# Kernel tuning notes

Hardware: AMD Instinct MI355X
Metric: run time of the kernel (lower is better)

The kernel has to match this reference:

```python
import jax, jax.numpy as jnp
import numpy as np

QK_DIM = 1024
V_DIM = 1024
NUM_HEADS = 16
HEAD_DIM = 64
INNER = NUM_HEADS * HEAD_DIM  # 1024
SCALE = HEAD_DIM ** -0.5


def setup_inputs() -> dict:
    key = jax.random.key(0)
    ks = jax.random.split(key, 8)
    m, nq, nkv = 4, 2048, 2048
    xq = jax.random.normal(ks[0], (m, nq, QK_DIM), dtype=jnp.float32)
    xk = jax.random.normal(ks[1], (m, nkv, QK_DIM), dtype=jnp.float32)
    xv = jax.random.normal(ks[2], (m, nkv, V_DIM), dtype=jnp.float32)
    # torch nn.Linear weights are [out, in]; y = x @ W.T
    s_qk = (QK_DIM) ** -0.5
    s_in = (INNER) ** -0.5
    Wq = jax.random.uniform(ks[3], (INNER, QK_DIM), jnp.float32, -s_qk, s_qk)
    Wk = jax.random.uniform(ks[4], (INNER, QK_DIM), jnp.float32, -s_qk, s_qk)
    Wv = jax.random.uniform(ks[5], (INNER, V_DIM), jnp.float32, -s_qk, s_qk)
    Wo = jax.random.uniform(ks[6], (V_DIM, INNER), jnp.float32, -s_in, s_in)
    bo = jax.random.uniform(ks[7], (V_DIM,), jnp.float32, -s_in, s_in)
    return {"xq": xq, "xk": xk, "xv": xv, "Wq": Wq, "Wk": Wk, "Wv": Wv, "Wo": Wo, "bo": bo}


def reference(xq, xk, xv, Wq, Wk, Wv, Wo, bo):
    m, nq, _ = xq.shape
    nkv = xk.shape[1]
    # projections (no bias), split heads: b n (h d) -> b h n d
    q = (xq @ Wq.T).reshape(m, nq, NUM_HEADS, HEAD_DIM).transpose(0, 2, 1, 3)
    k = (xk @ Wk.T).reshape(m, nkv, NUM_HEADS, HEAD_DIM).transpose(0, 2, 1, 3)
    v = (xv @ Wv.T).reshape(m, nkv, NUM_HEADS, HEAD_DIM).transpose(0, 2, 1, 3)
    dots = jnp.einsum("bhqd,bhkd->bhqk", q, k) * SCALE  # [m,h,nq,nkv]
    attn = jax.nn.softmax(dots, axis=-1)
    out = jnp.einsum("bhqk,bhkd->bhqd", attn, v)
    out = out.transpose(0, 2, 1, 3).reshape(m, nq, INNER)  # b h n d -> b n (h d)
    return out @ Wo.T + bo  # to_out Linear (dropout p=0 -> identity)
```

## Files before the change

kernel.cpp:

```cpp
#include <hip/hip_runtime.h>

typedef unsigned short u16;
using bf16x8 = __attribute__((ext_vector_type(8))) __bf16;
using f32x4  = __attribute__((ext_vector_type(4))) float;

#define QSCALE 0.18033688011f

#define EXP2F(x) __builtin_amdgcn_exp2f(x)
#define SCHED_FENCE() __builtin_amdgcn_sched_barrier(0)

__device__ __forceinline__ u16 f2bf(float f) {
  union { float f; unsigned int u; } x; x.f = f;
  unsigned int r = x.u + 0x7FFFu + ((x.u >> 16) & 1u);
  return (u16)(r >> 16);
}

__device__ __forceinline__ bf16x8 ld8(const u16* p) {
  return *reinterpret_cast<const bf16x8*>(p);
}

__device__ __forceinline__ void gload16(const void* g, void* l) {
  __builtin_amdgcn_global_load_lds(
      (const __attribute__((address_space(1))) unsigned int*)g,
      (__attribute__((address_space(3))) unsigned int*)l, 16, 0, 0);
}

__global__ void cast3_f32_to_bf16(const float* __restrict__ a, const float* __restrict__ b,
                                  const float* __restrict__ c, u16* __restrict__ out, int n4) {
  const int y = blockIdx.y;
  const int i = blockIdx.x * 256 + threadIdx.x;
  if (i >= n4) return;
  const float* src = (y == 0) ? a : (y == 1) ? b : c;
  const float4 v = reinterpret_cast<const float4*>(src)[i];
  ushort4 o;
  o.x = f2bf(v.x); o.y = f2bf(v.y); o.z = f2bf(v.z); o.w = f2bf(v.w);
  reinterpret_cast<ushort4*>(out + (size_t)y * n4 * 4)[i] = o;
}

__global__ void cast4_f32_to_bf16(const float* __restrict__ a, const float* __restrict__ b,
                                  const float* __restrict__ c, const float* __restrict__ d,
                                  u16* __restrict__ out, int n4) {
  const int y = blockIdx.y;
  const int i = blockIdx.x * 256 + threadIdx.x;
  if (i >= n4) return;
  const float* src = (y == 0) ? a : (y == 1) ? b : (y == 2) ? c : d;
  const float4 v = reinterpret_cast<const float4*>(src)[i];
  ushort4 o;
  o.x = f2bf(v.x); o.y = f2bf(v.y); o.z = f2bf(v.z); o.w = f2bf(v.w);
  reinterpret_cast<ushort4*>(out + (size_t)y * n4 * 4)[i] = o;
}

#define GEMM_CORE(A_, B_, K_, BX_, BY_)                                              \
  __shared__ alignas(16) u16 lds_a[128 * 32];                                        \
  __shared__ alignas(16) u16 lds_b[128 * 32];                                        \
  const int t = threadIdx.x;                                                         \
  const int w = t >> 6, lane = t & 63;                                               \
  const int wr = w >> 1, wc = w & 1;                                                 \
  const size_t row0 = (size_t)(BY_) * 128;                                           \
  const size_t col0 = (size_t)(BX_) * 128;                                           \
  f32x4 acc[4][4];                                                                   \
  _Pragma("unroll") for (int i = 0; i < 4; ++i)                                      \
    _Pragma("unroll") for (int j = 0; j < 4; ++j) acc[i][j] = {0.f, 0.f, 0.f, 0.f};  \
  const u16* ga = A_ + (row0 + (t >> 2)) * K_ + (t & 3) * 8;                         \
  const u16* gb = B_ + (col0 + (t >> 2)) * K_ + (t & 3) * 8;                         \
  u16* la = lds_a + w * 512;                                                         \
  u16* lb = lds_b + w * 512;                                                         \
  const int fr = lane & 15;                                                          \
  const int fk = (lane >> 4) * 8;                                                    \
  for (int kt = 0; kt < K_; kt += 32) {                                              \
    __syncthreads();                                                                 \
    gload16(ga + kt, la);                                                            \
    gload16(ga + (size_t)64 * K_ + kt, la + 2048);                                   \
    gload16(gb + kt, lb);                                                            \
    gload16(gb + (size_t)64 * K_ + kt, lb + 2048);                                   \
    asm volatile("s_waitcnt vmcnt(0)" ::: "memory");                                 \
    __syncthreads();                                                                 \
    bf16x8 af[4], bfr[4];                                                            \
    _Pragma("unroll") for (int i = 0; i < 4; ++i)                                    \
      af[i] = ld8(&lds_a[(wr * 64 + i * 16 + fr) * 32 + fk]);                        \
    _Pragma("unroll") for (int j = 0; j < 4; ++j)                                    \
      bfr[j] = ld8(&lds_b[(wc * 64 + j * 16 + fr) * 32 + fk]);                       \
    _Pragma("unroll") for (int i = 0; i < 4; ++i)                                    \
      _Pragma("unroll") for (int j = 0; j < 4; ++j)                                  \
        acc[i][j] = __builtin_amdgcn_mfma_f32_16x16x32_bf16(af[i], bfr[j], acc[i][j], 0, 0, 0); \
  }                                                                                  \
  const int er = (lane >> 4) * 4, ec = lane & 15;

__device__ __forceinline__ void gemm8b_core(const u16* __restrict__ A, const u16* __restrict__ B,
                                            int by, int bx, f32x4 (&acc)[4][4],
                                            u16 (*lds_a)[8192], u16 (*lds_b)[16384]) {
  const int t = threadIdx.x;
  const int w = t >> 6, lane = t & 63;
  const int wm = w >> 2, wn = w & 3;
  const int fr = lane & 15, lh = lane >> 4;
  const int xr = (fr & 4) << 2;
  const int kch = ((t & 7) ^ ((t >> 4) & 2)) * 8;

  const u16* ga = A + (size_t)(by * 128 + (t >> 3)) * 1024 + kch;
  const u16* gb = B + (size_t)(bx * 256 + (t >> 3)) * 1024 + kch;

#pragma unroll
  for (int m = 0; m < 4; ++m)
#pragma unroll
    for (int n = 0; n < 4; ++n) acc[m][n] = {0.f, 0.f, 0.f, 0.f};

#pragma unroll
  for (int q = 0; q < 2; ++q)
    gload16(ga + (size_t)q * 64 * 1024, &lds_a[0][q * 4096 + w * 512]);
#pragma unroll
  for (int q = 0; q < 4; ++q)
    gload16(gb + (size_t)q * 64 * 1024, &lds_b[0][q * 4096 + w * 512]);

  for (int it = 0; it < 8; ++it) {
    const int ts = 2 * it + 1;
    const int tn = (2 * it + 2) & 15;
    bf16x8 bfr[4][2];
#pragma unroll
    for (int p = 0; p < 8; ++p) {
      const int b = p >> 2, q = p & 3;
      if (q == 0) { asm volatile("s_waitcnt vmcnt(0)" ::: "memory"); }
      __builtin_amdgcn_s_barrier();
      if (q == 0) {
#pragma unroll
        for (int nn = 0; nn < 4; ++nn)
#pragma unroll
          for (int ks = 0; ks < 2; ++ks)
            bfr[nn][ks] = ld8(&lds_b[b][(wn * 64 + nn * 16 + fr) * 64 + ((ks * 32 + lh * 8) ^ xr)]);
      }
      bf16x8 af[2];
#pragma unroll
      for (int ks = 0; ks < 2; ++ks)
        af[ks] = ld8(&lds_a[b][(wm * 64 + q * 16 + fr) * 64 + ((ks * 32 + lh * 8) ^ xr)]);
      {
        const int tt = (p < 4) ? ts : tn;
        const int db = (p < 4) ? 1 : 0;
        if (q == 0) {
          gload16(gb + (size_t)0 * 64 * 1024 + tt * 64, &lds_b[db][0 * 4096 + w * 512]);
          gload16(gb + (size_t)1 * 64 * 1024 + tt * 64, &lds_b[db][1 * 4096 + w * 512]);
        } else if (q == 1) {
          gload16(gb + (size_t)2 * 64 * 1024 + tt * 64, &lds_b[db][2 * 4096 + w * 512]);
          gload16(gb + (size_t)3 * 64 * 1024 + tt * 64, &lds_b[db][3 * 4096 + w * 512]);
        } else if (q == 2) {
          gload16(ga + (size_t)0 * 64 * 1024 + tt * 64, &lds_a[db][0 * 4096 + w * 512]);
        } else {
          gload16(ga + (size_t)1 * 64 * 1024 + tt * 64, &lds_a[db][1 * 4096 + w * 512]);
        }
      }
      __builtin_amdgcn_s_setprio(1);
#pragma unroll
      for (int nn = 0; nn < 4; ++nn)
#pragma unroll
        for (int ks = 0; ks < 2; ++ks)
          acc[q][nn] = __builtin_amdgcn_mfma_f32_16x16x32_bf16(af[ks], bfr[nn][ks], acc[q][nn], 0, 0, 0);
      __builtin_amdgcn_s_setprio(0);
    }
  }
}

__global__ __launch_bounds__(512)
void gemm8_qkv(const u16* __restrict__ Aall, const u16* __restrict__ Ball,
               u16* __restrict__ Call) {
  __shared__ alignas(16) u16 lds_a[2][8192];
  __shared__ alignas(16) u16 lds_b[2][16384];
  const int g = (blockIdx.x & 7) * 96 + (blockIdx.x >> 3);
  const int z = g >> 8, r8 = g & 255;
  const int by = r8 >> 2, bx = r8 & 3;
  const u16* A = Aall + (size_t)z * 8192 * 1024;
  const u16* B = Ball + (size_t)z * 1024 * 1024;
  u16* C = Call + (size_t)z * 8192 * 1024;

  f32x4 acc[4][4];
  gemm8b_core(A, B, by, bx, acc, lds_a, lds_b);

  const int t = threadIdx.x;
  const int w = t >> 6, lane = t & 63;
  const int wm = w >> 2, wn = w & 3;
  const int er = (lane >> 4) * 4, ec = lane & 15;
#pragma unroll
  for (int m = 0; m < 4; ++m)
#pragma unroll
    for (int nn = 0; nn < 4; ++nn) {
      const size_t row = (size_t)by * 128 + wm * 64 + m * 16 + er;
      const size_t col = (size_t)bx * 256 + wn * 64 + nn * 16 + ec;
      if (z == 0) {
#pragma unroll
        for (int rr = 0; rr < 4; ++rr)
          C[(row + rr) * 1024 + col] = f2bf(acc[m][nn][rr] * QSCALE);
      } else if (z == 1) {
#pragma unroll
        for (int rr = 0; rr < 4; ++rr) {
          const size_t n = row + rr;
          const size_t colswz = (col & ~(size_t)63) | ((col & 63) ^ ((n & 7) << 3));
          C[n * 1024 + colswz] = f2bf(acc[m][nn][rr]);
        }
      } else {
        ushort4 o4;
        o4.x = f2bf(acc[m][nn][0]); o4.y = f2bf(acc[m][nn][1]);
        o4.z = f2bf(acc[m][nn][2]); o4.w = f2bf(acc[m][nn][3]);
        const size_t nloc = row & 2047;
        const size_t d = col & 63;
        size_t pos = (nloc & ~(size_t)31) | (((nloc >> 2) & 3) << 3) |
                     (((nloc >> 4) & 1) << 2) | (nloc & 3);
        pos ^= (d & 7) << 3;
        const size_t idx = (((row >> 11) * 16 + (col >> 6)) * 64 + d) * 2048 + pos;
        *reinterpret_cast<ushort4*>(&C[idx]) = o4;
      }
    }
}

__global__ __launch_bounds__(256)
void gemm_out(const u16* __restrict__ A, const u16* __restrict__ B,
              float* __restrict__ Cf, const float* __restrict__ bias) {
  const int g = (blockIdx.x & 7) * 64 + (blockIdx.x >> 3);
  const int bx = g & 7, by = g >> 3;
  GEMM_CORE(A, B, 1024, bx, by)
#pragma unroll
  for (int i = 0; i < 4; ++i)
#pragma unroll
    for (int j = 0; j < 4; ++j) {
      const size_t row = row0 + wr * 64 + i * 16 + er;
      const size_t col = col0 + wc * 64 + j * 16 + ec;
#pragma unroll
      for (int r = 0; r < 4; ++r)
        Cf[(row + r) * 1024 + col] = acc[i][j][r] + bias[col];
    }
}

__global__ __launch_bounds__(512)
void flash_attn(const u16* __restrict__ Q, const u16* __restrict__ Km,
                const u16* __restrict__ Vt, u16* __restrict__ O) {
  const int o_blk = (blockIdx.x & 7) * 64 + (blockIdx.x >> 3);
  const int qt = o_blk & 7, h = (o_blk >> 3) & 15, b = o_blk >> 7;
  const int t = threadIdx.x;
  const int w = t >> 6, lane = t & 63;
  const int l16 = lane & 15, lh = lane >> 4;

  __shared__ alignas(16) u16 kt_lds[2][64][64];
  __shared__ alignas(16) u16 vt_lds[2][64][64];

  const size_t base_qk = ((size_t)b * 2048) * 1024 + (size_t)h * 64;
  const size_t base_vt = ((size_t)(b * 16 + h)) * 64 * 2048;

  bf16x8 qf[2][2];
#pragma unroll
  for (int g = 0; g < 2; ++g) {
    const size_t qrow = (size_t)qt * 256 + (w * 2 + g) * 16 + l16;
    const u16* qp = Q + base_qk + qrow * 1024 + lh * 8;
    qf[g][0] = ld8(qp);
    qf[g][1] = ld8(qp + 32);
  }

  bf16x8 vones;
#pragma unroll
  for (int i = 0; i < 8; ++i) vones[i] = (__bf16)1.0f;

  f32x4 o_acc[2][4];
  f32x4 o_sum[2];
#pragma unroll
  for (int g = 0; g < 2; ++g) {
#pragma unroll
    for (int j = 0; j < 4; ++j) o_acc[g][j] = {0.f, 0.f, 0.f, 0.f};
    o_sum[g] = {0.f, 0.f, 0.f, 0.f};
  }

  const int srow = t >> 3;
  const int schk = (t & 7) * 8;
  const u16* kg = Km + base_qk + (size_t)srow * 1024 + schk;
  const u16* vg = Vt + base_vt + (size_t)srow * 2048 + schk;
  u16* kl0 = &kt_lds[0][0][0] + w * 512;
  u16* kl1 = &kt_lds[1][0][0] + w * 512;
  u16* vl0 = &vt_lds[0][0][0] + w * 512;
  u16* vl1 = &vt_lds[1][0][0] + w * 512;

  gload16(kg, kl0);
  gload16(vg, vl0);

  const int xo = (l16 & 7) << 3;

  for (int it = 0; it < 32; ++it) {
    const int cur = it & 1;
    asm volatile("s_waitcnt vmcnt(0)" ::: "memory");
    SCHED_FENCE();
    __syncthreads();
    SCHED_FENCE();

    if (it != 31) {
      const int nkv = (it + 1) * 64;
      gload16(kg + (size_t)nkv * 1024, cur ? kl0 : kl1);
      gload16(vg + nkv, cur ? vl0 : vl1);
    }
    SCHED_FENCE();

    f32x4 s[2][4];
#pragma unroll
    for (int g = 0; g < 2; ++g)
#pragma unroll
      for (int j = 0; j < 4; ++j) s[g][j] = {0.f, 0.f, 0.f, 0.f};
    __builtin_amdgcn_s_setprio(1);
#pragma unroll
    for (int j = 0; j < 4; ++j)
#pragma unroll
      for (int ks = 0; ks < 2; ++ks) {
        bf16x8 kf = ld8(&kt_lds[cur][j * 16 + l16][(ks * 32 + lh * 8) ^ xo]);
        s[0][j] = __builtin_amdgcn_mfma_f32_16x16x32_bf16(kf, qf[0][ks], s[0][j], 0, 0, 0);
        s[1][j] = __builtin_amdgcn_mfma_f32_16x16x32_bf16(kf, qf[1][ks], s[1][j], 0, 0, 0);
      }
    __builtin_amdgcn_s_setprio(0);

    bf16x8 pa[2][2];
#pragma unroll
    for (int g = 0; g < 2; ++g)
#pragma unroll
      for (int j = 0; j < 4; ++j)
#pragma unroll
        for (int r = 0; r < 4; ++r)
          s[g][j][r] = EXP2F(s[g][j][r]);
#pragma unroll
    for (int g = 0; g < 2; ++g)
#pragma unroll
      for (int c = 0; c < 2; ++c)
#pragma unroll
        for (int i = 0; i < 8; ++i)
          pa[g][c][i] = (__bf16)s[g][2 * c + (i >> 2)][i & 3];

    __builtin_amdgcn_s_setprio(1);
#pragma unroll
    for (int c = 0; c < 2; ++c) {
      o_sum[0] = __builtin_amdgcn_mfma_f32_16x16x32_bf16(pa[0][c], vones, o_sum[0], 0, 0, 0);
      o_sum[1] = __builtin_amdgcn_mfma_f32_16x16x32_bf16(pa[1][c], vones, o_sum[1], 0, 0, 0);
#pragma unroll
      for (int jd = 0; jd < 4; ++jd) {
        bf16x8 vf = ld8(&vt_lds[cur][jd * 16 + l16][(c * 32 + lh * 8) ^ xo]);
        o_acc[0][jd] = __builtin_amdgcn_mfma_f32_16x16x32_bf16(pa[0][c], vf, o_acc[0][jd], 0, 0, 0);
        o_acc[1][jd] = __builtin_amdgcn_mfma_f32_16x16x32_bf16(pa[1][c], vf, o_acc[1][jd], 0, 0, 0);
      }
    }
    __builtin_amdgcn_s_setprio(0);
  }

#pragma unroll
  for (int g = 0; g < 2; ++g) {
    float linv[4];
#pragma unroll
    for (int r = 0; r < 4; ++r) linv[r] = 1.0f / o_sum[g][r];
    const size_t orow0 = (size_t)b * 2048 + (size_t)qt * 256 + (w * 2 + g) * 16;
#pragma unroll
    for (int jd = 0; jd < 4; ++jd) {
      const int col = h * 64 + jd * 16 + l16;
#pragma unroll
      for (int r = 0; r < 4; ++r)
        O[(orow0 + lh * 4 + r) * 1024 + col] = f2bf(o_acc[g][jd][r] * linv[r]);
    }
  }
}

extern "C" void kernel_launch(void* const* d_in, const int* in_sizes, int n_in,
                              void* d_out, int out_size, void* d_ws, size_t ws_size,
                              hipStream_t stream) {
  const float* xq = (const float*)d_in[0];
  const float* xk = (const float*)d_in[1];
  const float* xv = (const float*)d_in[2];
  const float* Wq = (const float*)d_in[3];
  const float* Wk = (const float*)d_in[4];
  const float* Wv = (const float*)d_in[5];
  const float* Wo = (const float*)d_in[6];
  const float* bo = (const float*)d_in[7];
  float* out = (float*)d_out;

  const size_t X = (size_t)8192 * 1024;
  const size_t W = (size_t)1024 * 1024;

  u16* p = (u16*)d_ws;
  u16* x_bf  = p; p += 3 * X;
  u16* w_bf  = p; p += 4 * W;
  u16* qkv   = p; p += 3 * X;
  u16* attn_bf = x_bf;

  dim3 blk(256);
  cast3_f32_to_bf16<<<dim3(8192, 3), blk, 0, stream>>>(xq, xk, xv, x_bf, (int)(X / 4));
  cast4_f32_to_bf16<<<dim3(1024, 4), blk, 0, stream>>>(Wq, Wk, Wv, Wo, w_bf, (int)(W / 4));

  gemm8_qkv<<<dim3(768), dim3(512), 0, stream>>>(x_bf, w_bf, qkv);

  flash_attn<<<dim3(512), dim3(512), 0, stream>>>(qkv, qkv + X, qkv + 2 * X, attn_bf);

  gemm_out<<<dim3(512), blk, 0, stream>>>(attn_bf, w_bf + 3 * W, out, bo);
}
```

Before: 197.7 us.

## Switch QKV GEMM to triple-buffered LDS pipeline with two tiles in flight

Replaces the double-buffered, interleaved-load schedule in the QKV projection GEMM with a three-stage LDS ring buffer. Each k-tile's six global-to-LDS loads are issued together two tiles ahead, and a partial vmcnt wait lets the next tile's loads remain outstanding. The aim is to hide global memory latency better and drop the full vmcnt(0) drain every two tiles. In exchange, LDS use rises from 96KB to 144KB per block, which can reduce occupancy, and barriers are still taken per quarter-step.

```diff
diff --git a/kernel.cpp b/kernel.cpp
--- a/kernel.cpp
+++ b/kernel.cpp
@@ -86,7 +86,7 @@
   }                                                                                  \
   const int er = (lane >> 4) * 4, ec = lane & 15;
 
-__device__ __forceinline__ void gemm8b_core(const u16* __restrict__ A, const u16* __restrict__ B,
+__device__ __forceinline__ void gemm8c_core(const u16* __restrict__ A, const u16* __restrict__ B,
                                             int by, int bx, f32x4 (&acc)[4][4],
                                             u16 (*lds_a)[8192], u16 (*lds_b)[16384]) {
   const int t = threadIdx.x;
@@ -104,48 +104,42 @@
 #pragma unroll
     for (int n = 0; n < 4; ++n) acc[m][n] = {0.f, 0.f, 0.f, 0.f};
 
-#pragma unroll
-  for (int q = 0; q < 2; ++q)
-    gload16(ga + (size_t)q * 64 * 1024, &lds_a[0][q * 4096 + w * 512]);
-#pragma unroll
-  for (int q = 0; q < 4; ++q)
-    gload16(gb + (size_t)q * 64 * 1024, &lds_b[0][q * 4096 + w * 512]);
-
-  for (int it = 0; it < 8; ++it) {
-    const int ts = 2 * it + 1;
-    const int tn = (2 * it + 2) & 15;
+#define STAGE6(tile, buf)                                                      \
+  do {                                                                         \
+    gload16(ga + (size_t)0 * 65536 + (tile) * 64, &lds_a[buf][0 * 4096 + w * 512]); \
+    gload16(ga + (size_t)1 * 65536 + (tile) * 64, &lds_a[buf][1 * 4096 + w * 512]); \
+    gload16(gb + (size_t)0 * 65536 + (tile) * 64, &lds_b[buf][0 * 4096 + w * 512]); \
+    gload16(gb + (size_t)1 * 65536 + (tile) * 64, &lds_b[buf][1 * 4096 + w * 512]); \
+    gload16(gb + (size_t)2 * 65536 + (tile) * 64, &lds_b[buf][2 * 4096 + w * 512]); \
+    gload16(gb + (size_t)3 * 65536 + (tile) * 64, &lds_b[buf][3 * 4096 + w * 512]); \
+  } while (0)
+
+  STAGE6(0, 0);
+  STAGE6(1, 1);
+
+  int buf = 0;
+  int sbuf = 2;
+  for (int kt = 0; kt < 16; ++kt) {
+    if (kt < 15) { asm volatile("s_waitcnt vmcnt(6)" ::: "memory"); }
+    else         { asm volatile("s_waitcnt vmcnt(0)" ::: "memory"); }
+    __builtin_amdgcn_s_barrier();
+    SCHED_FENCE();
+    if (kt < 14) STAGE6(kt + 2, sbuf);
+    SCHED_FENCE();
+
     bf16x8 bfr[4][2];
 #pragma unroll
-    for (int p = 0; p < 8; ++p) {
-      const int b = p >> 2, q = p & 3;
-      if (q == 0) { asm volatile("s_waitcnt vmcnt(0)" ::: "memory"); }
-      __builtin_amdgcn_s_barrier();
-      if (q == 0) {
-#pragma unroll
-        for (int nn = 0; nn < 4; ++nn)
-#pragma unroll
-          for (int ks = 0; ks < 2; ++ks)
-            bfr[nn][ks] = ld8(&lds_b[b][(wn * 64 + nn * 16 + fr) * 64 + ((ks * 32 + lh * 8) ^ xr)]);
-      }
+    for (int nn = 0; nn < 4; ++nn)
+#pragma unroll
+      for (int ks = 0; ks < 2; ++ks)
+        bfr[nn][ks] = ld8(&lds_b[buf][(wn * 64 + nn * 16 + fr) * 64 + ((ks * 32 + lh * 8) ^ xr)]);
+#pragma unroll
+    for (int q = 0; q < 4; ++q) {
+      if (q) __builtin_amdgcn_s_barrier();
       bf16x8 af[2];
 #pragma unroll
       for (int ks = 0; ks < 2; ++ks)
-        af[ks] = ld8(&lds_a[b][(wm * 64 + q * 16 + fr) * 64 + ((ks * 32 + lh * 8) ^ xr)]);
-      {
-        const int tt = (p < 4) ? ts : tn;
-        const int db = (p < 4) ? 1 : 0;
-        if (q == 0) {
-          gload16(gb + (size_t)0 * 64 * 1024 + tt * 64, &lds_b[db][0 * 4096 + w * 512]);
-          gload16(gb + (size_t)1 * 64 * 1024 + tt * 64, &lds_b[db][1 * 4096 + w * 512]);
-        } else if (q == 1) {
-          gload16(gb + (size_t)2 * 64 * 1024 + tt * 64, &lds_b[db][2 * 4096 + w * 512]);
-          gload16(gb + (size_t)3 * 64 * 1024 + tt * 64, &lds_b[db][3 * 4096 + w * 512]);
-        } else if (q == 2) {
-          gload16(ga + (size_t)0 * 64 * 1024 + tt * 64, &lds_a[db][0 * 4096 + w * 512]);
-        } else {
-          gload16(ga + (size_t)1 * 64 * 1024 + tt * 64, &lds_a[db][1 * 4096 + w * 512]);
-        }
-      }
+        af[ks] = ld8(&lds_a[buf][(wm * 64 + q * 16 + fr) * 64 + ((ks * 32 + lh * 8) ^ xr)]);
       __builtin_amdgcn_s_setprio(1);
 #pragma unroll
       for (int nn = 0; nn < 4; ++nn)
@@ -154,14 +148,17 @@
           acc[q][nn] = __builtin_amdgcn_mfma_f32_16x16x32_bf16(af[ks], bfr[nn][ks], acc[q][nn], 0, 0, 0);
       __builtin_amdgcn_s_setprio(0);
     }
-  }
+    buf = (buf == 2) ? 0 : buf + 1;
+    sbuf = (sbuf == 2) ? 0 : sbuf + 1;
+  }
+#undef STAGE6
 }
 
 __global__ __launch_bounds__(512)
 void gemm8_qkv(const u16* __restrict__ Aall, const u16* __restrict__ Ball,
                u16* __restrict__ Call) {
-  __shared__ alignas(16) u16 lds_a[2][8192];
-  __shared__ alignas(16) u16 lds_b[2][16384];
+  __shared__ alignas(16) u16 lds_a[3][8192];
+  __shared__ alignas(16) u16 lds_b[3][16384];
   const int g = (blockIdx.x & 7) * 96 + (blockIdx.x >> 3);
   const int z = g >> 8, r8 = g & 255;
   const int by = r8 >> 2, bx = r8 & 3;
@@ -170,7 +167,7 @@
   u16* C = Call + (size_t)z * 8192 * 1024;
 
   f32x4 acc[4][4];
-  gemm8b_core(A, B, by, bx, acc, lds_a, lds_b);
+  gemm8c_core(A, B, by, bx, acc, lds_a, lds_b);
 
   const int t = threadIdx.x;
   const int w = t >> 6, lane = t & 63;
```

Measured after the change: 198.9 us. About the same (+0.6%).
